# Performance work log

Measured on AMD Instinct MI355X. Metric: run time of the kernel, lower is better.

## Reference

```python
import jax, jax.numpy as jnp
import numpy as np

B, F, E, A = 2048, 64, 32, 4  # batch, features, embedding, attention_factor

def setup_inputs() -> dict:
    key = jax.random.key(0)
    k = jax.random.split(key, 6)
    return {
        "x": jax.random.normal(k[0], (B, F, E), dtype=jnp.float32),
        "attn_w": jax.random.normal(k[1], (E, A), dtype=jnp.float32) * (1.0 / np.sqrt(E)),
        "attn_b": jnp.zeros((A,), dtype=jnp.float32),
        "attn_h": jax.random.normal(k[2], (A, 1), dtype=jnp.float32) * (1.0 / np.sqrt(A)),
        "pool_w": jax.random.normal(k[3], (E, 1), dtype=jnp.float32) * (1.0 / np.sqrt(E)),
        "pool_b": jnp.zeros((1,), dtype=jnp.float32),
    }

def reference(x, attn_w, attn_b, attn_h, pool_w, pool_b):
    Fdim = x.shape[1]
    iu, ju = np.triu_indices(Fdim, k=1)  # pair indices i<j, P = F*(F-1)/2
    # pairwise element-wise products: [B, P, E]
    pairs = x[:, iu, :] * x[:, ju, :]
    # attention MLP: relu(pairs @ W + b) @ h -> [B, P, 1]
    dense = jax.nn.relu(jnp.einsum('bpe,ea->bpa', pairs, attn_w) + attn_b)
    scores = jnp.einsum('bpa,ao->bpo', dense, attn_h)
    attn = jax.nn.softmax(scores, axis=1)  # softmax over pair axis
    # softmax-weighted sum pooling over pairs -> [B, E]
    reduced = jnp.sum(attn * pairs, axis=1)
    # final dense to scalar (dropout is identity at inference)
    return reduced @ pool_w + pool_b  # [B, 1]
```

## Files before the change

### kernel.cpp

```cpp
#include <hip/hip_runtime.h>

typedef _Float16 f16x8 __attribute__((ext_vector_type(8)));
typedef _Float16 f16x4 __attribute__((ext_vector_type(4)));
typedef float    f32x4 __attribute__((ext_vector_type(4)));

#define FDIM 64
#define EDIM 32
#define ADIM 4
#define XH_S 40

__device__ __constant__ int TBASE_host_unused[4] = {0, 4, 7, 9};

__global__ __launch_bounds__(256, 3)
void afm_kernel(const float* __restrict__ x,
                const float* __restrict__ attn_w,
                const float* __restrict__ attn_b,
                const float* __restrict__ attn_h,
                const float* __restrict__ pool_w,
                const float* __restrict__ pool_b,
                float* __restrict__ out)
{
    __shared__ _Float16 Xh[4][FDIM * XH_S];
    __shared__ _Float16 Wh[ADIM * EDIM];
    __shared__ _Float16 Pwh[EDIM];

    const int tid  = threadIdx.x;
    const int wave = tid >> 6;
    const int lane = tid & 63;
    const int n16  = lane & 15;
    const int q    = lane >> 4;

    const int batch = blockIdx.x * 4 + wave;
    const float* xb = x + (size_t)batch * (FDIM * EDIM);
    _Float16* xh = Xh[wave];

    #pragma unroll
    for (int k = 0; k < 8; ++k) {
        int idx = lane + 64 * k;
        float4 v = ((const float4*)xb)[idx];
        int row = idx >> 3, c4 = idx & 7;
        f16x4 hv = {(_Float16)v.x, (_Float16)v.y, (_Float16)v.z, (_Float16)v.w};
        *(f16x4*)&xh[row * XH_S + c4 * 4] = hv;
    }
    if (tid < ADIM * EDIM) {
        int a = tid >> 5, e = tid & 31;
        Wh[a * EDIM + e] = (_Float16)attn_w[e * ADIM + a];
    } else if (tid < ADIM * EDIM + EDIM) {
        int e = tid - ADIM * EDIM;
        Pwh[e] = (_Float16)pool_w[e];
    }
    float hb[ADIM], hh[ADIM];
    #pragma unroll
    for (int a = 0; a < ADIM; ++a) { hb[a] = attn_b[a]; hh[a] = attn_h[a]; }
    __syncthreads();

    f16x8 bfrag[4], wfrag[4];
    #pragma unroll
    for (int ct = 0; ct < 4; ++ct)
        bfrag[ct] = *(const f16x8*)&xh[(ct * 16 + n16) * XH_S + q * 8];
    #pragma unroll
    for (int a = 0; a < ADIM; ++a)
        wfrag[a] = *(const f16x8*)&Wh[a * EDIM + q * 8];
    f16x8 pwf = *(const f16x8*)&Pwh[q * 8];

    float val[10][4];
    #pragma unroll
    for (int t = 0; t < 10; ++t)
        #pragma unroll
        for (int r = 0; r < 4; ++r) val[t][r] = 0.f;

    const int tbase[4] = {0, 4, 7, 9};
    #pragma unroll
    for (int mt = 0; mt < 4; ++mt) {
        f16x8 xa = *(const f16x8*)&xh[(mt * 16 + n16) * XH_S + q * 8];
        #pragma unroll
        for (int a = 0; a < ADIM; ++a) {
            f16x8 ya = xa * wfrag[a];
            #pragma unroll
            for (int nt = mt; nt < 4; ++nt) {
                f32x4 z = {0.f, 0.f, 0.f, 0.f};
                f32x4 acc = __builtin_amdgcn_mfma_f32_16x16x32_f16(ya, bfrag[nt], z, 0, 0, 0);
                int t = tbase[mt] + (nt - mt);
                #pragma unroll
                for (int r = 0; r < 4; ++r)
                    val[t][r] += fmaxf(acc[r] + hb[a], 0.f) * hh[a];
            }
        }
    }

    float M = -3e38f;
    #pragma unroll
    for (int mt = 0; mt < 4; ++mt)
        #pragma unroll
        for (int nt = mt; nt < 4; ++nt) {
            int t = tbase[mt] + (nt - mt);
            #pragma unroll
            for (int r = 0; r < 4; ++r) {
                bool valid = (nt > mt) || ((q * 4 + r) < n16);
                if (valid) M = fmaxf(M, val[t][r]);
            }
        }
    #pragma unroll
    for (int off = 32; off >= 1; off >>= 1)
        M = fmaxf(M, __shfl_xor(M, off));

    float psum = 0.f;
    #pragma unroll
    for (int mt = 0; mt < 4; ++mt)
        #pragma unroll
        for (int nt = mt; nt < 4; ++nt) {
            int t = tbase[mt] + (nt - mt);
            #pragma unroll
            for (int r = 0; r < 4; ++r) {
                bool valid = (nt > mt) || ((q * 4 + r) < n16);
                float p = valid ? __expf(val[t][r] - M) : 0.f;
                val[t][r] = p;
                psum += p;
            }
        }

    float dot = 0.f;
    #pragma unroll
    for (int mt = 0; mt < 4; ++mt) {
        f16x8 xa = *(const f16x8*)&xh[(mt * 16 + n16) * XH_S + q * 8];
        f16x8 yp = xa * pwf;
        #pragma unroll
        for (int nt = mt; nt < 4; ++nt) {
            f32x4 z = {0.f, 0.f, 0.f, 0.f};
            f32x4 g = __builtin_amdgcn_mfma_f32_16x16x32_f16(yp, bfrag[nt], z, 0, 0, 0);
            int t = tbase[mt] + (nt - mt);
            #pragma unroll
            for (int r = 0; r < 4; ++r)
                dot += val[t][r] * g[r];
        }
    }

    #pragma unroll
    for (int off = 32; off >= 1; off >>= 1) {
        dot  += __shfl_xor(dot, off);
        psum += __shfl_xor(psum, off);
    }
    if (lane == 0)
        out[batch] = dot / psum + pool_b[0];
}

extern "C" void kernel_launch(void* const* d_in, const int* in_sizes, int n_in,
                              void* d_out, int out_size, void* d_ws, size_t ws_size,
                              hipStream_t stream) {
    const float* x      = (const float*)d_in[0];
    const float* attn_w = (const float*)d_in[1];
    const float* attn_b = (const float*)d_in[2];
    const float* attn_h = (const float*)d_in[3];
    const float* pool_w = (const float*)d_in[4];
    const float* pool_b = (const float*)d_in[5];
    float* out = (float*)d_out;
    int B = in_sizes[0] / (FDIM * EDIM);
    afm_kernel<<<B / 4, 256, 0, stream>>>(x, attn_w, attn_b, attn_h, pool_w, pool_b, out);
}
```

Measured before the change: 75.58 us.

## Split each batch's pair tiles across four waves with cross-wave softmax merge

Each block now handles a single batch row instead of four. The ten upper-triangular 16x16 pair tiles are spread over the four waves (3,3,2,2), and per-wave max, sum and dot partials are merged through shared memory with an online-softmax rescale. The goal is more parallelism, with 2048 blocks instead of 512, plus lower register pressure and a higher occupancy hint. The cost is an extra block-wide barrier and uneven work across waves.

```diff
diff --git a/kernel.cpp b/kernel.cpp
--- a/kernel.cpp
+++ b/kernel.cpp
@@ -9,9 +9,8 @@
 #define ADIM 4
 #define XH_S 40
 
-__device__ __constant__ int TBASE_host_unused[4] = {0, 4, 7, 9};
 
-__global__ __launch_bounds__(256, 3)
+__global__ __launch_bounds__(256, 4)
 void afm_kernel(const float* __restrict__ x,
                 const float* __restrict__ attn_w,
                 const float* __restrict__ attn_b,
@@ -20,9 +19,10 @@
                 const float* __restrict__ pool_b,
                 float* __restrict__ out)
 {
-    __shared__ _Float16 Xh[4][FDIM * XH_S];
+    __shared__ _Float16 Xh[FDIM * XH_S];
     __shared__ _Float16 Wh[ADIM * EDIM];
     __shared__ _Float16 Pwh[EDIM];
+    __shared__ float    red[4][3];
 
     const int tid  = threadIdx.x;
     const int wave = tid >> 6;
@@ -30,17 +30,16 @@
     const int n16  = lane & 15;
     const int q    = lane >> 4;
 
-    const int batch = blockIdx.x * 4 + wave;
+    const int batch = blockIdx.x;
     const float* xb = x + (size_t)batch * (FDIM * EDIM);
-    _Float16* xh = Xh[wave];
 
     #pragma unroll
-    for (int k = 0; k < 8; ++k) {
-        int idx = lane + 64 * k;
+    for (int k = 0; k < 2; ++k) {
+        int idx = tid + 256 * k;
         float4 v = ((const float4*)xb)[idx];
         int row = idx >> 3, c4 = idx & 7;
         f16x4 hv = {(_Float16)v.x, (_Float16)v.y, (_Float16)v.z, (_Float16)v.w};
-        *(f16x4*)&xh[row * XH_S + c4 * 4] = hv;
+        *(f16x4*)&Xh[row * XH_S + c4 * 4] = hv;
     }
     if (tid < ADIM * EDIM) {
         int a = tid >> 5, e = tid & 31;
@@ -54,84 +53,88 @@
     for (int a = 0; a < ADIM; ++a) { hb[a] = attn_b[a]; hh[a] = attn_h[a]; }
     __syncthreads();
 
-    f16x8 bfrag[4], wfrag[4];
+    const int NT = (wave < 2) ? 3 : 2;
+    int mt_[3], nt_[3], diag_[3];
     #pragma unroll
-    for (int ct = 0; ct < 4; ++ct)
-        bfrag[ct] = *(const f16x8*)&xh[(ct * 16 + n16) * XH_S + q * 8];
+    for (int tt = 0; tt < 3; ++tt) {
+        int t = wave + 4 * tt;
+        mt_[tt]  = (int)((0x3221110000ULL >> (4 * t)) & 0xF);
+        nt_[tt]  = (int)((0x3323213210ULL >> (4 * t)) & 0xF);
+        diag_[tt] = (mt_[tt] == nt_[tt]);
+    }
+
+    f16x8 wfrag[ADIM];
     #pragma unroll
     for (int a = 0; a < ADIM; ++a)
         wfrag[a] = *(const f16x8*)&Wh[a * EDIM + q * 8];
     f16x8 pwf = *(const f16x8*)&Pwh[q * 8];
 
-    float val[10][4];
+    f16x8 fa[3], fb[3];
+    float val[3][4];
     #pragma unroll
-    for (int t = 0; t < 10; ++t)
+    for (int tt = 0; tt < 3; ++tt) {
         #pragma unroll
-        for (int r = 0; r < 4; ++r) val[t][r] = 0.f;
+        for (int r = 0; r < 4; ++r) val[tt][r] = 0.f;
+        if (tt < NT) {
+            fa[tt] = *(const f16x8*)&Xh[(mt_[tt] * 16 + n16) * XH_S + q * 8];
+            fb[tt] = *(const f16x8*)&Xh[(nt_[tt] * 16 + n16) * XH_S + q * 8];
+        }
+    }
 
-    const int tbase[4] = {0, 4, 7, 9};
     #pragma unroll
-    for (int mt = 0; mt < 4; ++mt) {
-        f16x8 xa = *(const f16x8*)&xh[(mt * 16 + n16) * XH_S + q * 8];
-        #pragma unroll
-        for (int a = 0; a < ADIM; ++a) {
-            f16x8 ya = xa * wfrag[a];
+    for (int tt = 0; tt < 3; ++tt) {
+        if (tt < NT) {
             #pragma unroll
-            for (int nt = mt; nt < 4; ++nt) {
+            for (int a = 0; a < ADIM; ++a) {
+                f16x8 ya = fa[tt] * wfrag[a];
                 f32x4 z = {0.f, 0.f, 0.f, 0.f};
-                f32x4 acc = __builtin_amdgcn_mfma_f32_16x16x32_f16(ya, bfrag[nt], z, 0, 0, 0);
-                int t = tbase[mt] + (nt - mt);
+                f32x4 acc = __builtin_amdgcn_mfma_f32_16x16x32_f16(ya, fb[tt], z, 0, 0, 0);
                 #pragma unroll
                 for (int r = 0; r < 4; ++r)
-                    val[t][r] += fmaxf(acc[r] + hb[a], 0.f) * hh[a];
+                    val[tt][r] += fmaxf(acc[r] + hb[a], 0.f) * hh[a];
             }
         }
     }
 
     float M = -3e38f;
     #pragma unroll
-    for (int mt = 0; mt < 4; ++mt)
-        #pragma unroll
-        for (int nt = mt; nt < 4; ++nt) {
-            int t = tbase[mt] + (nt - mt);
+    for (int tt = 0; tt < 3; ++tt) {
+        if (tt < NT) {
             #pragma unroll
             for (int r = 0; r < 4; ++r) {
-                bool valid = (nt > mt) || ((q * 4 + r) < n16);
-                if (valid) M = fmaxf(M, val[t][r]);
+                bool valid = !diag_[tt] || ((q * 4 + r) < n16);
+                if (valid) M = fmaxf(M, val[tt][r]);
             }
         }
+    }
     #pragma unroll
     for (int off = 32; off >= 1; off >>= 1)
         M = fmaxf(M, __shfl_xor(M, off));
 
     float psum = 0.f;
     #pragma unroll
-    for (int mt = 0; mt < 4; ++mt)
-        #pragma unroll
-        for (int nt = mt; nt < 4; ++nt) {
-            int t = tbase[mt] + (nt - mt);
+    for (int tt = 0; tt < 3; ++tt) {
+        if (tt < NT) {
             #pragma unroll
             for (int r = 0; r < 4; ++r) {
-                bool valid = (nt > mt) || ((q * 4 + r) < n16);
-                float p = valid ? __expf(val[t][r] - M) : 0.f;
-                val[t][r] = p;
+                bool valid = !diag_[tt] || ((q * 4 + r) < n16);
+                float p = valid ? __expf(val[tt][r] - M) : 0.f;
+                val[tt][r] = p;
                 psum += p;
             }
         }
+    }
 
     float dot = 0.f;
     #pragma unroll
-    for (int mt = 0; mt < 4; ++mt) {
-        f16x8 xa = *(const f16x8*)&xh[(mt * 16 + n16) * XH_S + q * 8];
-        f16x8 yp = xa * pwf;
-        #pragma unroll
-        for (int nt = mt; nt < 4; ++nt) {
+    for (int tt = 0; tt < 3; ++tt) {
+        if (tt < NT) {
+            f16x8 yp = fa[tt] * pwf;
             f32x4 z = {0.f, 0.f, 0.f, 0.f};
-            f32x4 g = __builtin_amdgcn_mfma_f32_16x16x32_f16(yp, bfrag[nt], z, 0, 0, 0);
-            int t = tbase[mt] + (nt - mt);
+            f32x4 g = __builtin_amdgcn_mfma_f32_16x16x32_f16(yp, fb[tt], z, 0, 0, 0);
             #pragma unroll
             for (int r = 0; r < 4; ++r)
-                dot += val[t][r] * g[r];
+                dot += val[tt][r] * g[r];
         }
     }
 
@@ -140,8 +143,24 @@
         dot  += __shfl_xor(dot, off);
         psum += __shfl_xor(psum, off);
     }
-    if (lane == 0)
-        out[batch] = dot / psum + pool_b[0];
+    if (lane == 0) {
+        red[wave][0] = M;
+        red[wave][1] = psum;
+        red[wave][2] = dot;
+    }
+    __syncthreads();
+
+    if (tid == 0) {
+        float Mg = fmaxf(fmaxf(red[0][0], red[1][0]), fmaxf(red[2][0], red[3][0]));
+        float den = 0.f, num = 0.f;
+        #pragma unroll
+        for (int w = 0; w < 4; ++w) {
+            float s = __expf(red[w][0] - Mg);
+            den += red[w][1] * s;
+            num += red[w][2] * s;
+        }
+        out[batch] = num / den + pool_b[0];
+    }
 }
 
 extern "C" void kernel_launch(void* const* d_in, const int* in_sizes, int n_in,
@@ -155,5 +174,5 @@
     const float* pool_b = (const float*)d_in[5];
     float* out = (float*)d_out;
     int B = in_sizes[0] / (FDIM * EDIM);
-    afm_kernel<<<B / 4, 256, 0, stream>>>(x, attn_w, attn_b, attn_h, pool_w, pool_b, out);
+    afm_kernel<<<B, 256, 0, stream>>>(x, attn_w, attn_b, attn_h, pool_w, pool_b, out);
 }
```

Result: no change. 75.04 us (-0.7%).
